# Kernel tuning notes

Measured on AMD Instinct MI355X. Metric: run time of the kernel, lower is better.

The kernel has to match this reference:

```python
import jax, jax.numpy as jnp
import numpy as np

B, T, D_MODEL, N_HEADS = 2, 2048, 2048, 16
D_HEAD = D_MODEL // N_HEADS
SCALE = 1.0 / np.sqrt(D_HEAD)


def setup_inputs() -> dict:
    key = jax.random.key(0)
    ks = jax.random.split(key, 5)
    w_std = 1.0 / np.sqrt(D_MODEL)
    x = jax.random.normal(ks[0], (B, T, D_MODEL), dtype=jnp.float32)
    W_q = jax.random.normal(ks[1], (D_MODEL, D_MODEL), dtype=jnp.float32) * w_std
    W_k = jax.random.normal(ks[2], (D_MODEL, D_MODEL), dtype=jnp.float32) * w_std
    W_v = jax.random.normal(ks[3], (D_MODEL, D_MODEL), dtype=jnp.float32) * w_std
    W_o = jax.random.normal(ks[4], (D_MODEL, D_MODEL), dtype=jnp.float32) * w_std
    return {"x": x, "W_q": W_q, "W_k": W_k, "W_v": W_v, "W_o": W_o}


def _split_heads(y):
    # [B, T, D] -> [B, H, T, d_head]
    b, t, _ = y.shape
    return y.reshape(b, t, N_HEADS, D_HEAD).transpose(0, 2, 1, 3)


def reference(x, W_q, W_k, W_v, W_o):
    # Linear layers (torch nn.Linear: y = x @ W.T)
    Q = _split_heads(x @ W_q.T)
    K = _split_heads(x @ W_k.T)
    V = _split_heads(x @ W_v.T)
    # Causal softmax attention (math-equivalent to the tiled online-softmax loop)
    scores = jnp.einsum('bhqd,bhkd->bhqk', Q, K) * SCALE
    causal_mask = jnp.tril(jnp.ones((T, T), dtype=bool))  # [T, T]
    scores = jnp.where(causal_mask, scores, -jnp.inf)
    P = jax.nn.softmax(scores, axis=-1)
    O = jnp.einsum('bhqk,bhkd->bhqd', P, V)
    out = O.transpose(0, 2, 1, 3).reshape(B, T, D_MODEL)  # merge heads
    return out @ W_o.T
```

## Files before the change

kernel.cpp:

```cpp
#include <hip/hip_runtime.h>
#include <hip/hip_bf16.h>
#include <hip/hip_fp16.h>

#define B_   2
#define T_   2048
#define DM   2048
#define NH   16
#define DH   128
#define M_   (B_*T_)
#define SCALE_ 0.08838834764831845f

typedef _Float16 f16;
typedef f16  half8 __attribute__((ext_vector_type(8)));
typedef f16  half4 __attribute__((ext_vector_type(4)));
typedef float f32x4 __attribute__((ext_vector_type(4)));

#define GL16(gp, lp) __builtin_amdgcn_global_load_lds( \
    (const __attribute__((address_space(1))) void*)(gp), \
    (__attribute__((address_space(3))) void*)(lp), 16, 0, 0)

#define MFMA16(a, b, c) __builtin_amdgcn_mfma_f32_16x16x32_f16((a), (b), (c), 0, 0, 0)

struct CvtArgs { const float* s[5]; f16* d[5]; };

__global__ __launch_bounds__(256) void convert_all(CvtArgs a) {
    size_t i4 = (size_t)blockIdx.x * 256 + threadIdx.x;
    int r; size_t off;
    if (i4 < 2097152) { r = 0; off = i4; }
    else { size_t k = i4 - 2097152; r = 1 + (int)(k >> 20); off = k & 1048575; }
    float4 v = *((const float4*)a.s[r] + off);
    half4 h;
    h[0] = (f16)v.x; h[1] = (f16)v.y; h[2] = (f16)v.z; h[3] = (f16)v.w;
    *((half4*)a.d[r] + off) = h;
}

#define NT_K 32

__global__ __launch_bounds__(512, 2)
void qkv3(const f16* __restrict__ A, const f16* __restrict__ Bw,
          f16* __restrict__ dst)
{
    __shared__ __align__(16) char smem[114688];

    const int tid  = threadIdx.x;
    const int lane = tid & 63;
    const int w    = tid >> 6;
    const int wr   = w >> 1, wc = w & 1;

    const int id = (blockIdx.x & 7) * 64 + (blockIdx.x >> 3);
    const int bm = id & 15, bn = id >> 4;
    const int m0 = bm * 256, n0 = bn * 192;

    const int scol8 = (((tid & 7) ^ ((tid >> 3) & 7)) << 3);
    const int rc0 = (((lane >> 4) * 16)      ) ^ ((lane & 7) << 4);
    const int rc1 = (64 + (lane >> 4) * 16   ) ^ ((lane & 7) << 4);

    f32x4 acc[4][6] = {};

#define QSTAGE_A(bufb, ch, s, kt) GL16( \
    A + (size_t)(m0 + (ch)*128 + (tid>>8)*64 + (s)*32 + ((tid>>3)&31)) * 2048 + (kt)*64 + scol8, \
    smem + (bufb)*57344 + (ch)*16384 + (s)*8192 + w*1024)
#define QSTAGE_B(bufb, u, kt) GL16( \
    Bw + (size_t)(n0 + (tid>>7)*48 + (u)*16 + ((tid>>3)&15)) * 2048 + (kt)*64 + scol8, \
    smem + (bufb)*57344 + 32768 + (u)*8192 + w*1024)

    const int abase = (wr >> 1) * 16384 + (wr & 1) * 4096 + (lane & 15) * 128;
    const int bbase = 32768 + wc * 4096 + (lane & 15) * 128;

    half8 af0[4][2], af1[4][2], bnx[2];

    QSTAGE_A(0, 0, 0, 0); QSTAGE_A(0, 0, 1, 0);
    QSTAGE_A(0, 1, 0, 0); QSTAGE_A(0, 1, 1, 0);
    QSTAGE_B(0, 0, 0);    QSTAGE_B(0, 1, 0);    QSTAGE_B(0, 2, 0);
    {
        asm volatile("s_waitcnt vmcnt(2)" ::: "memory");
        __builtin_amdgcn_s_barrier();
        __builtin_amdgcn_sched_barrier(0);
        const char* buf0 = smem;
        #pragma unroll
        for (int m = 0; m < 4; ++m) {
            const char* p = buf0 + (m >> 1) * 8192 + abase + (m & 1) * 2048;
            af0[m][0] = *(const half8*)(p + rc0);
            af0[m][1] = *(const half8*)(p + rc1);
        }
        bnx[0] = *(const half8*)(buf0 + bbase + rc0);
        bnx[1] = *(const half8*)(buf0 + bbase + rc1);
    }

#define GATE(n_) do { \
    asm volatile("s_waitcnt vmcnt(" #n_ ")" ::: "memory"); \
    __builtin_amdgcn_s_barrier(); \
    __builtin_amdgcn_sched_barrier(0); \
} while (0)

#define MFC(AF, BB, f_) do { \
    __builtin_amdgcn_s_setprio(1); \
    _Pragma("unroll") \
    for (int m_ = 0; m_ < 4; ++m_) { \
        acc[m_][f_] = MFMA16(AF[m_][0], (BB)[0], acc[m_][f_]); \
        acc[m_][f_] = MFMA16(AF[m_][1], (BB)[1], acc[m_][f_]); \
    } \
    __builtin_amdgcn_s_setprio(0); \
} while (0)

#define RDB(dstv, off) do { \
    const char* p_ = buf + bbase + (off); \
    dstv[0] = *(const half8*)(p_ + rc0); \
    dstv[1] = *(const half8*)(p_ + rc1); \
} while (0)

#define BODY(t_, c_, AFC, AFN) do { \
    const char* buf  = smem + (c_) * 57344; \
    const char* nbuf = smem + ((c_) ^ 1) * 57344; \
    const int  kt    = ((t_) + 1 < NT_K) ? (t_) + 1 : (t_); \
    half8 b3[2], b1[2], b4[2], b2[2], b5[2]; \
     \
    RDB(b3, 2048); \
    QSTAGE_A((c_) ^ 1, 0, 0, kt); QSTAGE_A((c_) ^ 1, 0, 1, kt); \
    MFC(AFC, bnx, 0); \
     \
    GATE(3); \
    RDB(b1, 8192); \
    QSTAGE_A((c_) ^ 1, 1, 0, kt); QSTAGE_A((c_) ^ 1, 1, 1, kt); \
    MFC(AFC, b3, 3); \
     \
    RDB(b4, 8192 + 2048); \
    QSTAGE_B((c_) ^ 1, 0, kt); \
    MFC(AFC, b1, 1); \
     \
    GATE(5); \
    RDB(b2, 16384); \
    QSTAGE_B((c_) ^ 1, 1, kt); \
    MFC(AFC, b4, 4); \
     \
    GATE(1); \
    RDB(b5, 16384 + 2048); \
    { const char* p_ = nbuf + abase; \
      AFN[0][0] = *(const half8*)(p_ + rc0); \
      AFN[0][1] = *(const half8*)(p_ + rc1); \
      AFN[1][0] = *(const half8*)(p_ + 2048 + rc0); \
      AFN[1][1] = *(const half8*)(p_ + 2048 + rc1); } \
    QSTAGE_B((c_) ^ 1, 2, kt); \
    MFC(AFC, b2, 2); \
     \
    { const char* p_ = nbuf + 8192 + abase; \
      AFN[2][0] = *(const half8*)(p_ + rc0); \
      AFN[2][1] = *(const half8*)(p_ + rc1); \
      AFN[3][0] = *(const half8*)(p_ + 2048 + rc0); \
      AFN[3][1] = *(const half8*)(p_ + 2048 + rc1); } \
    { const char* p_ = nbuf + bbase; \
      bnx[0] = *(const half8*)(p_ + rc0); \
      bnx[1] = *(const half8*)(p_ + rc1); } \
    MFC(AFC, b5, 5); \
} while (0)

    for (int t = 0; t < NT_K; t += 2) {
        BODY(t,     0, af0, af1);
        BODY(t + 1, 1, af1, af0);
    }
#undef BODY
#undef RDB
#undef MFC
#undef GATE
#undef QSTAGE_A
#undef QSTAGE_B

    asm volatile("s_waitcnt vmcnt(0)" ::: "memory");

    #pragma unroll
    for (int m = 0; m < 4; ++m)
        #pragma unroll
        for (int f = 0; f < 6; ++f)
            #pragma unroll
            for (int j = 0; j < 4; ++j) {
                int row  = m0 + wr * 64 + m * 16 + (lane >> 4) * 4 + j;
                int gcol = n0 + wc * 96 + f * 16 + (lane & 15);
                int sec = gcol >> 11, cic = gcol & 2047;
                int b = row >> 11, tt = row & (T_ - 1);
                int h = cic >> 7, d = cic & 127;
                float cs = (sec == 0) ? SCALE_ : 1.0f;
                dst[(size_t)sec * ((size_t)M_ * 2048) +
                    ((size_t)(b * NH + h) * T_ + tt) * DH + d] = (f16)(acc[m][f][j] * cs);
            }
}

#define NT_W 32

__global__ __launch_bounds__(512, 2)
void wo2(const f16* __restrict__ A, const f16* __restrict__ Bw,
         float* __restrict__ Cf)
{
    __shared__ __align__(16) char smem[98304];

    const int tid  = threadIdx.x;
    const int lane = tid & 63;
    const int w    = tid >> 6;
    const int wr   = w >> 1, wc = w & 1;

    const int id = (blockIdx.x & 7) * 32 + (blockIdx.x >> 3);
    const int bm = id & 15, bn = id >> 4;
    const int m0 = bm * 256, n0 = bn * 128;

    const int scol8 = (((tid & 7) ^ ((tid >> 3) & 7)) << 3);
    const int rc0 = (((lane >> 4) * 16)      ) ^ ((lane & 7) << 4);
    const int rc1 = (64 + (lane >> 4) * 16   ) ^ ((lane & 7) << 4);

    f32x4 acc[4][4] = {};

#define WSA(bufb, s, kt) GL16( \
    A + (size_t)(m0 + ((s)&1)*128 + (tid>>8)*64 + ((s)>>1)*32 + ((tid>>3)&31)) * 2048 + (kt)*64 + scol8, \
    smem + (bufb)*49152 + (s)*8192 + w*1024)
#define WSB(bufb, u, kt) GL16( \
    Bw + (size_t)(n0 + (tid>>8)*64 + (u)*32 + ((tid>>3)&31)) * 2048 + (kt)*64 + scol8, \
    smem + (bufb)*49152 + 32768 + (u)*8192 + w*1024)

    WSA(0, 0, 0); WSA(0, 1, 0); WSB(0, 0, 0); WSB(0, 1, 0);
    WSA(0, 2, 0); WSA(0, 3, 0);

    const int abase = (wr >> 1) * 8192 + (wr & 1) * 4096 + (lane & 15) * 128;
    const int bbase = 32768 + wc * 4096 + (lane & 15) * 128;

#define WGATE(n_) do { \
    asm volatile("s_waitcnt vmcnt(" #n_ ")" ::: "memory"); \
    __builtin_amdgcn_s_barrier(); \
    __builtin_amdgcn_sched_barrier(0); \
} while (0)

    for (int t = 0; t < NT_W; ++t) {
        const int c = t & 1;
        const char* buf = smem + c * 49152;
        const int kt = (t + 1 < NT_W) ? t + 1 : t;

        half8 af[4][2], bf[4][2];

        WGATE(2);
        #pragma unroll
        for (int m = 0; m < 2; ++m) {
            const char* p = buf + abase + m * 2048;
            af[m][0] = *(const half8*)(p + rc0);
            af[m][1] = *(const half8*)(p + rc1);
        }
        #pragma unroll
        for (int n = 0; n < 4; ++n) {
            const char* p = buf + bbase + (n >> 1) * 8192 + (n & 1) * 2048;
            bf[n][0] = *(const half8*)(p + rc0);
            bf[n][1] = *(const half8*)(p + rc1);
        }
        WSA(c ^ 1, 0, kt); WSA(c ^ 1, 1, kt);
        WSB(c ^ 1, 0, kt); WSB(c ^ 1, 1, kt);
        __builtin_amdgcn_s_setprio(1);
        #pragma unroll
        for (int m = 0; m < 2; ++m)
            #pragma unroll
            for (int n = 0; n < 4; ++n) {
                acc[m][n] = MFMA16(af[m][0], bf[n][0], acc[m][n]);
                acc[m][n] = MFMA16(af[m][1], bf[n][1], acc[m][n]);
            }
        __builtin_amdgcn_s_setprio(0);

        WGATE(4);
        #pragma unroll
        for (int m = 2; m < 4; ++m) {
            const char* p = buf + 16384 + abase + (m & 1) * 2048;
            af[m][0] = *(const half8*)(p + rc0);
            af[m][1] = *(const half8*)(p + rc1);
        }
        WSA(c ^ 1, 2, kt); WSA(c ^ 1, 3, kt);
        __builtin_amdgcn_s_setprio(1);
        #pragma unroll
        for (int m = 2; m < 4; ++m)
            #pragma unroll
            for (int n = 0; n < 4; ++n) {
                acc[m][n] = MFMA16(af[m][0], bf[n][0], acc[m][n]);
                acc[m][n] = MFMA16(af[m][1], bf[n][1], acc[m][n]);
            }
        __builtin_amdgcn_s_setprio(0);
    }
#undef WGATE
#undef WSA
#undef WSB

    asm volatile("s_waitcnt vmcnt(0)" ::: "memory");

    #pragma unroll
    for (int m = 0; m < 4; ++m)
        #pragma unroll
        for (int n = 0; n < 4; ++n)
            #pragma unroll
            for (int j = 0; j < 4; ++j) {
                int row = m0 + wr * 64 + m * 16 + (lane >> 4) * 4 + j;
                int col = n0 + wc * 64 + n * 16 + (lane & 15);
                Cf[(size_t)row * 2048 + col] = acc[m][n][j];
            }
}

__global__ __launch_bounds__(256)
void vtrans(const f16* __restrict__ Vin, f16* __restrict__ Vout)
{
    __shared__ f16 ld[64][72];
    const int tid = threadIdx.x;
    const int dd = blockIdx.x;
    const int tt = blockIdx.y;
    const int bh = blockIdx.z;

    const int r  = tid >> 2;
    const int s2 = (tid & 3) * 2;

    const f16* src = Vin + ((size_t)bh * T_ + tt * 64 + r) * DH + dd * 64;
    half8 v0 = *(const half8*)(src + s2 * 8);
    half8 v1 = *(const half8*)(src + s2 * 8 + 8);
    #pragma unroll
    for (int e = 0; e < 8; ++e) ld[s2 * 8 + e][r]     = v0[e];
    #pragma unroll
    for (int e = 0; e < 8; ++e) ld[s2 * 8 + 8 + e][r] = v1[e];
    __syncthreads();

    f16* dst = Vout + ((size_t)bh * DH + dd * 64 + r) * T_ + tt * 64;
    *(half8*)(dst + s2 * 8)     = *(const half8*)&ld[r][s2 * 8];
    *(half8*)(dst + s2 * 8 + 8) = *(const half8*)&ld[r][s2 * 8 + 8];
}

#define QB 64
#define KB 64
#define PP 72
#define NQT (T_/QB)

__global__ __launch_bounds__(256, 2)
void attn_fwd(const f16* __restrict__ Q, const f16* __restrict__ K,
              const f16* __restrict__ Vt, f16* __restrict__ O)
{
    __shared__ __align__(16) char Ks[2][16384];
    __shared__ __align__(16) char Vs[2][16384];
    __shared__ __align__(16) f16 Ps[4][16][PP];

    const int tid  = threadIdx.x;
    const int lane = tid & 63;
    const int w    = tid >> 6;
    const int g    = lane >> 4;

    const int bid  = blockIdx.x;
    const int swz  = (bid & 7) * 64 + (bid >> 3);
    const int bh   = swz >> 4;
    const int pair = swz & 15;
    const size_t base = (size_t)bh * T_ * DH;
    const int b = bh >> 4, h = bh & 15;

    const int krow0 = w * 4 + g;
    const int kswz  = ((lane & 15) ^ (krow0 & 7)) << 3;
    const int vrow0 = w * 8 + (lane >> 3);
    const int vswz  = (((lane & 7) ^ ((lane >> 3) & 7)) << 3);

#define STAGE_K(c_, kv) do { \
    _Pragma("unroll") for (int i_ = 0; i_ < 4; ++i_) { \
        const f16* g_ = K + base + (size_t)((kv) + i_*16 + krow0) * DH + kswz; \
        GL16(g_, &Ks[c_][i_*4096 + w*1024]); } } while (0)
#define STAGE_V(c_, kv) do { \
    _Pragma("unroll") for (int i_ = 0; i_ < 4; ++i_) { \
        const f16* g_ = Vt + base + (size_t)(i_*32 + vrow0) * T_ + (kv) + vswz; \
        GL16(g_, &Vs[c_][i_*4096 + w*1024]); } } while (0)

#define QKT(SA, QF) do { \
    __builtin_amdgcn_s_setprio(1); \
    _Pragma("unroll") \
    for (int n_ = 0; n_ < 4; ++n_) \
        _Pragma("unroll") \
        for (int kk_ = 0; kk_ < 4; ++kk_) { \
            half8 kfv = *(const half8*)(kb + (n_*16 + (lane & 15)) * 256 + \
                ((kk_*32 + g * 8) * 2 ^ ((lane & 7) << 4))); \
            SA[n_] = MFMA16(kfv, QF[kk_], SA[n_]); \
        } \
    __builtin_amdgcn_s_setprio(0); \
} while (0)

#define SMAX(SA, MRUN, LSUM, OO) do { \
    float mx_ = SA[0][0]; \
    _Pragma("unroll") \
    for (int n_ = 0; n_ < 4; ++n_) \
        _Pragma("unroll") \
        for (int j_ = 0; j_ < 4; ++j_) mx_ = fmaxf(mx_, SA[n_][j_]); \
    mx_ = fmaxf(mx_, __shfl_xor(mx_, 16)); \
    mx_ = fmaxf(mx_, __shfl_xor(mx_, 32)); \
    if (!__all(mx_ <= MRUN + 5.f)) { \
        float mnew_ = fmaxf(MRUN, mx_); \
        float sf_ = __expf(MRUN - mnew_); \
        _Pragma("unroll") \
        for (int nn_ = 0; nn_ < 8; ++nn_) OO[nn_] *= sf_; \
        LSUM *= sf_; \
        MRUN = mnew_; \
    } \
    float rs_ = 0.f; \
    _Pragma("unroll") \
    for (int n_ = 0; n_ < 4; ++n_) \
        _Pragma("unroll") \
        for (int j_ = 0; j_ < 4; ++j_) { \
            float p_ = __expf(SA[n_][j_] - MRUN); \
            SA[n_][j_] = p_; \
            rs_ += p_; \
        } \
    LSUM += rs_; \
} while (0)

#define PFRAG(SA, BP) do { \
    _Pragma("unroll") \
    for (int n_ = 0; n_ < 4; ++n_) { \
        half4 hv_; \
        hv_[0] = (f16)SA[n_][0]; hv_[1] = (f16)SA[n_][1]; \
        hv_[2] = (f16)SA[n_][2]; hv_[3] = (f16)SA[n_][3]; \
        *reinterpret_cast<half4*>(&Ps[w][lane & 15][n_*16 + g*4]) = hv_; \
    } \
    _Pragma("unroll") \
    for (int cc_ = 0; cc_ < 2; ++cc_) \
        BP[cc_] = *reinterpret_cast<const half8*>(&Ps[w][lane & 15][cc_*32 + g*8]); \
} while (0)

#define PV(OO, BP) do { \
    __builtin_amdgcn_s_setprio(1); \
    _Pragma("unroll") \
    for (int n_ = 0; n_ < 8; ++n_) \
        _Pragma("unroll") \
        for (int cc_ = 0; cc_ < 2; ++cc_) { \
            half8 vf_ = *(const half8*)(vb + (n_*16 + (lane & 15)) * 128 + \
                ((cc_*64 + g*16) ^ ((lane & 7) << 4))); \
            OO[n_] = MFMA16(vf_, BP[cc_], OO[n_]); \
        } \
    __builtin_amdgcn_s_setprio(0); \
} while (0)

    const int qt1 = pair;
    const int qt2 = NQT - 1 - pair;
    const int nt1 = qt1 + 1;
    const int ntU = qt2 + 1;
    const int qg1 = qt1 * QB + w * 16 + (lane & 15);
    const int qg2 = qt2 * QB + w * 16 + (lane & 15);

    half8 qf1[4], qf2[4];
    #pragma unroll
    for (int kk = 0; kk < 4; ++kk) {
        qf1[kk] = *reinterpret_cast<const half8*>(
            &Q[base + (size_t)qg1 * DH + kk * 32 + g * 8]);
        qf2[kk] = *reinterpret_cast<const half8*>(
            &Q[base + (size_t)qg2 * DH + kk * 32 + g * 8]);
    }

    float mrun1 = -1e30f, lsum1 = 0.f;
    float mrun2 = -1e30f, lsum2 = 0.f;
    f32x4 o1[8] = {};
    f32x4 o2[8] = {};

    STAGE_K(0, 0);
    STAGE_V(0, 0);

    for (int it = 0; it < ntU; ++it) {
        const int c = it & 1;
        __syncthreads();
        if (it + 1 < ntU) {
            STAGE_K(c ^ 1, (it + 1) * KB);
            STAGE_V(c ^ 1, (it + 1) * KB);
        }
        const bool s1 = (it < nt1);
        const char* kb = &Ks[c][0];
        const char* vb = &Vs[c][0];

        f32x4 sa2[4] = {};
        f32x4 sa1[4] = {};

        QKT(sa2, qf2);
        if (s1) QKT(sa1, qf1);

        if (it == ntU - 1) {
            #pragma unroll
            for (int n = 0; n < 4; ++n)
                #pragma unroll
                for (int j = 0; j < 4; ++j) {
                    int kg = it * KB + n*16 + g*4 + j;
                    if (kg > qg2) sa2[n][j] = -1e30f;
                }
        }
        if (s1 && it == nt1 - 1) {
            #pragma unroll
            for (int n = 0; n < 4; ++n)
                #pragma unroll
                for (int j = 0; j < 4; ++j) {
                    int kg = it * KB + n*16 + g*4 + j;
                    if (kg > qg1) sa1[n][j] = -1e30f;
                }
        }

        SMAX(sa2, mrun2, lsum2, o2);
        half8 bp2[2];
        PFRAG(sa2, bp2);
        PV(o2, bp2);

        if (s1) {
            SMAX(sa1, mrun1, lsum1, o1);
            half8 bp1[2];
            PFRAG(sa1, bp1);
            PV(o1, bp1);
        }
    }

    {
        float l2 = lsum2;
        l2 += __shfl_xor(l2, 16);
        l2 += __shfl_xor(l2, 32);
        float invl = 1.0f / l2;
        #pragma unroll
        for (int n = 0; n < 8; ++n) {
            half4 hv;
            hv[0] = (f16)(o2[n][0] * invl); hv[1] = (f16)(o2[n][1] * invl);
            hv[2] = (f16)(o2[n][2] * invl); hv[3] = (f16)(o2[n][3] * invl);
            *reinterpret_cast<half4*>(
                &O[((size_t)(b * T_ + qg2) * NH + h) * DH + n*16 + g*4]) = hv;
        }
    }
    {
        float l1 = lsum1;
        l1 += __shfl_xor(l1, 16);
        l1 += __shfl_xor(l1, 32);
        float invl = 1.0f / l1;
        #pragma unroll
        for (int n = 0; n < 8; ++n) {
            half4 hv;
            hv[0] = (f16)(o1[n][0] * invl); hv[1] = (f16)(o1[n][1] * invl);
            hv[2] = (f16)(o1[n][2] * invl); hv[3] = (f16)(o1[n][3] * invl);
            *reinterpret_cast<half4*>(
                &O[((size_t)(b * T_ + qg1) * NH + h) * DH + n*16 + g*4]) = hv;
        }
    }
#undef PV
#undef PFRAG
#undef SMAX
#undef QKT
#undef STAGE_K
#undef STAGE_V
}

extern "C" void kernel_launch(void* const* d_in, const int* in_sizes, int n_in,
                              void* d_out, int out_size, void* d_ws, size_t ws_size,
                              hipStream_t stream)
{
    const float* x  = (const float*)d_in[0];
    const float* wq = (const float*)d_in[1];
    const float* wk = (const float*)d_in[2];
    const float* wv = (const float*)d_in[3];
    const float* wo = (const float*)d_in[4];
    float* out = (float*)d_out;

    const size_t nx = (size_t)M_ * DM;
    const size_t nw = (size_t)DM * DM;
    const size_t need = (nx * 5 + nw * 4) * sizeof(f16);
    if (ws_size < need) return;

    char* ws = (char*)d_ws;
    f16* xh  = (f16*)ws;  ws += nx * 2;
    f16* wqh = (f16*)ws;  ws += nw * 2;
    f16* wkh = (f16*)ws;  ws += nw * 2;
    f16* wvh = (f16*)ws;  ws += nw * 2;
    f16* woh = (f16*)ws;  ws += nw * 2;
    f16* Qh  = (f16*)ws;  ws += nx * 2;
    f16* Kh  = (f16*)ws;  ws += nx * 2;
    f16* Vh  = (f16*)ws;  ws += nx * 2;
    f16* Oh  = (f16*)ws;  ws += nx * 2;

    f16* Vth = xh;

    CvtArgs ca;
    ca.s[0] = x;  ca.d[0] = xh;
    ca.s[1] = wq; ca.d[1] = wqh;
    ca.s[2] = wk; ca.d[2] = wkh;
    ca.s[3] = wv; ca.d[3] = wvh;
    ca.s[4] = wo; ca.d[4] = woh;
    convert_all<<<24576, 256, 0, stream>>>(ca);

    qkv3<<<dim3(512), 512, 0, stream>>>(xh, wqh, Qh);

    vtrans<<<dim3(2, 32, 32), 256, 0, stream>>>(Vh, Vth);

    attn_fwd<<<dim3(512), 256, 0, stream>>>(Qh, Kh, Vth, Oh);

    wo2<<<dim3(256), 512, 0, stream>>>(Oh, woh, out);
}
```

Before: 228.4 us.

## Share K/V LDS fragment loads across paired query tiles; shrink Wo GEMM tiles

In attention, the two query tiles handled by a block now share each K and V fragment read from LDS, issuing both MFMAs per load instead of reading the fragments twice. The Wo projection GEMM moves from 256x128 tiles with 512 threads to 128x128 tiles with 256 threads over 512 blocks, with smaller LDS buffers and adjusted wait counts. The attention change cuts LDS traffic but raises register pressure. The Wo change trades per-block reuse for more blocks and possibly higher occupancy.

```diff
diff --git a/kernel.cpp b/kernel.cpp
--- a/kernel.cpp
+++ b/kernel.cpp
@@ -186,20 +186,20 @@
 
 #define NT_W 32
 
-__global__ __launch_bounds__(512, 2)
+__global__ __launch_bounds__(256, 2)
 void wo2(const f16* __restrict__ A, const f16* __restrict__ Bw,
          float* __restrict__ Cf)
 {
-    __shared__ __align__(16) char smem[98304];
+    __shared__ __align__(16) char smem[65536];
 
     const int tid  = threadIdx.x;
     const int lane = tid & 63;
     const int w    = tid >> 6;
     const int wr   = w >> 1, wc = w & 1;
 
-    const int id = (blockIdx.x & 7) * 32 + (blockIdx.x >> 3);
-    const int bm = id & 15, bn = id >> 4;
-    const int m0 = bm * 256, n0 = bn * 128;
+    const int id = (blockIdx.x & 7) * 64 + (blockIdx.x >> 3);
+    const int bm = id & 31, bn = id >> 5;
+    const int m0 = bm * 128, n0 = bn * 128;
 
     const int scol8 = (((tid & 7) ^ ((tid >> 3) & 7)) << 3);
     const int rc0 = (((lane >> 4) * 16)      ) ^ ((lane & 7) << 4);
@@ -208,17 +208,18 @@
     f32x4 acc[4][4] = {};
 
 #define WSA(bufb, s, kt) GL16( \
-    A + (size_t)(m0 + ((s)&1)*128 + (tid>>8)*64 + ((s)>>1)*32 + ((tid>>3)&31)) * 2048 + (kt)*64 + scol8, \
-    smem + (bufb)*49152 + (s)*8192 + w*1024)
+    A + (size_t)(m0 + ((s)&1)*64 + ((s)>>1)*32 + (tid>>3)) * 2048 + (kt)*64 + scol8, \
+    smem + (bufb)*32768 + (s)*4096 + w*1024)
 #define WSB(bufb, u, kt) GL16( \
-    Bw + (size_t)(n0 + (tid>>8)*64 + (u)*32 + ((tid>>3)&31)) * 2048 + (kt)*64 + scol8, \
-    smem + (bufb)*49152 + 32768 + (u)*8192 + w*1024)
-
-    WSA(0, 0, 0); WSA(0, 1, 0); WSB(0, 0, 0); WSB(0, 1, 0);
+    Bw + (size_t)(n0 + ((u)&1)*64 + ((u)>>1)*32 + (tid>>3)) * 2048 + (kt)*64 + scol8, \
+    smem + (bufb)*32768 + 16384 + (u)*4096 + w*1024)
+
+    WSA(0, 0, 0); WSA(0, 1, 0);
+    WSB(0, 0, 0); WSB(0, 1, 0); WSB(0, 2, 0); WSB(0, 3, 0);
     WSA(0, 2, 0); WSA(0, 3, 0);
 
-    const int abase = (wr >> 1) * 8192 + (wr & 1) * 4096 + (lane & 15) * 128;
-    const int bbase = 32768 + wc * 4096 + (lane & 15) * 128;
+    const int abase = wr * 4096 + (lane & 15) * 128;
+    const int bbase = 16384 + wc * 4096 + (lane & 15) * 128;
 
 #define WGATE(n_) do { \
     asm volatile("s_waitcnt vmcnt(" #n_ ")" ::: "memory"); \
@@ -228,7 +229,7 @@
 
     for (int t = 0; t < NT_W; ++t) {
         const int c = t & 1;
-        const char* buf = smem + c * 49152;
+        const char* buf = smem + c * 32768;
         const int kt = (t + 1 < NT_W) ? t + 1 : t;
 
         half8 af[4][2], bf[4][2];
@@ -236,7 +237,7 @@
         WGATE(2);
         #pragma unroll
         for (int m = 0; m < 2; ++m) {
-            const char* p = buf + abase + m * 2048;
+            const char* p = buf + abase + (m & 1) * 2048;
             af[m][0] = *(const half8*)(p + rc0);
             af[m][1] = *(const half8*)(p + rc1);
         }
@@ -247,7 +248,7 @@
             bf[n][1] = *(const half8*)(p + rc1);
         }
         WSA(c ^ 1, 0, kt); WSA(c ^ 1, 1, kt);
-        WSB(c ^ 1, 0, kt); WSB(c ^ 1, 1, kt);
+        WSB(c ^ 1, 0, kt); WSB(c ^ 1, 1, kt); WSB(c ^ 1, 2, kt); WSB(c ^ 1, 3, kt);
         __builtin_amdgcn_s_setprio(1);
         #pragma unroll
         for (int m = 0; m < 2; ++m)
@@ -258,10 +259,10 @@
             }
         __builtin_amdgcn_s_setprio(0);
 
-        WGATE(4);
+        WGATE(6);
         #pragma unroll
         for (int m = 2; m < 4; ++m) {
-            const char* p = buf + 16384 + abase + (m & 1) * 2048;
+            const char* p = buf + 8192 + abase + (m & 1) * 2048;
             af[m][0] = *(const half8*)(p + rc0);
             af[m][1] = *(const half8*)(p + rc1);
         }
@@ -358,19 +359,6 @@
     _Pragma("unroll") for (int i_ = 0; i_ < 4; ++i_) { \
         const f16* g_ = Vt + base + (size_t)(i_*32 + vrow0) * T_ + (kv) + vswz; \
         GL16(g_, &Vs[c_][i_*4096 + w*1024]); } } while (0)
-
-#define QKT(SA, QF) do { \
-    __builtin_amdgcn_s_setprio(1); \
-    _Pragma("unroll") \
-    for (int n_ = 0; n_ < 4; ++n_) \
-        _Pragma("unroll") \
-        for (int kk_ = 0; kk_ < 4; ++kk_) { \
-            half8 kfv = *(const half8*)(kb + (n_*16 + (lane & 15)) * 256 + \
-                ((kk_*32 + g * 8) * 2 ^ ((lane & 7) << 4))); \
-            SA[n_] = MFMA16(kfv, QF[kk_], SA[n_]); \
-        } \
-    __builtin_amdgcn_s_setprio(0); \
-} while (0)
 
 #define SMAX(SA, MRUN, LSUM, OO) do { \
     float mx_ = SA[0][0]; \
@@ -413,19 +401,6 @@
         BP[cc_] = *reinterpret_cast<const half8*>(&Ps[w][lane & 15][cc_*32 + g*8]); \
 } while (0)
 
-#define PV(OO, BP) do { \
-    __builtin_amdgcn_s_setprio(1); \
-    _Pragma("unroll") \
-    for (int n_ = 0; n_ < 8; ++n_) \
-        _Pragma("unroll") \
-        for (int cc_ = 0; cc_ < 2; ++cc_) { \
-            half8 vf_ = *(const half8*)(vb + (n_*16 + (lane & 15)) * 128 + \
-                ((cc_*64 + g*16) ^ ((lane & 7) << 4))); \
-            OO[n_] = MFMA16(vf_, BP[cc_], OO[n_]); \
-        } \
-    __builtin_amdgcn_s_setprio(0); \
-} while (0)
-
     const int qt1 = pair;
     const int qt2 = NQT - 1 - pair;
     const int nt1 = qt1 + 1;
@@ -464,8 +439,28 @@
         f32x4 sa2[4] = {};
         f32x4 sa1[4] = {};
 
-        QKT(sa2, qf2);
-        if (s1) QKT(sa1, qf1);
+        __builtin_amdgcn_s_setprio(1);
+        if (s1) {
+            #pragma unroll
+            for (int n = 0; n < 4; ++n)
+                #pragma unroll
+                for (int kk = 0; kk < 4; ++kk) {
+                    half8 kfv = *(const half8*)(kb + (n*16 + (lane & 15)) * 256 +
+                        ((kk*32 + g * 8) * 2 ^ ((lane & 7) << 4)));
+                    sa2[n] = MFMA16(kfv, qf2[kk], sa2[n]);
+                    sa1[n] = MFMA16(kfv, qf1[kk], sa1[n]);
+                }
+        } else {
+            #pragma unroll
+            for (int n = 0; n < 4; ++n)
+                #pragma unroll
+                for (int kk = 0; kk < 4; ++kk) {
+                    half8 kfv = *(const half8*)(kb + (n*16 + (lane & 15)) * 256 +
+                        ((kk*32 + g * 8) * 2 ^ ((lane & 7) << 4)));
+                    sa2[n] = MFMA16(kfv, qf2[kk], sa2[n]);
+                }
+        }
+        __builtin_amdgcn_s_setprio(0);
 
         if (it == ntU - 1) {
             #pragma unroll
@@ -487,16 +482,35 @@
         }
 
         SMAX(sa2, mrun2, lsum2, o2);
-        half8 bp2[2];
-        PFRAG(sa2, bp2);
-        PV(o2, bp2);
-
+        half8 bp2[2], bp1[2];
         if (s1) {
             SMAX(sa1, mrun1, lsum1, o1);
-            half8 bp1[2];
             PFRAG(sa1, bp1);
-            PV(o1, bp1);
-        }
+        }
+        PFRAG(sa2, bp2);
+
+        __builtin_amdgcn_s_setprio(1);
+        if (s1) {
+            #pragma unroll
+            for (int n = 0; n < 8; ++n)
+                #pragma unroll
+                for (int cc = 0; cc < 2; ++cc) {
+                    half8 vf = *(const half8*)(vb + (n*16 + (lane & 15)) * 128 +
+                        ((cc*64 + g*16) ^ ((lane & 7) << 4)));
+                    o2[n] = MFMA16(vf, bp2[cc], o2[n]);
+                    o1[n] = MFMA16(vf, bp1[cc], o1[n]);
+                }
+        } else {
+            #pragma unroll
+            for (int n = 0; n < 8; ++n)
+                #pragma unroll
+                for (int cc = 0; cc < 2; ++cc) {
+                    half8 vf = *(const half8*)(vb + (n*16 + (lane & 15)) * 128 +
+                        ((cc*64 + g*16) ^ ((lane & 7) << 4)));
+                    o2[n] = MFMA16(vf, bp2[cc], o2[n]);
+                }
+        }
+        __builtin_amdgcn_s_setprio(0);
     }
 
     {
@@ -527,10 +541,8 @@
                 &O[((size_t)(b * T_ + qg1) * NH + h) * DH + n*16 + g*4]) = hv;
         }
     }
-#undef PV
 #undef PFRAG
 #undef SMAX
-#undef QKT
 #undef STAGE_K
 #undef STAGE_V
 }
@@ -578,5 +590,5 @@
 
     attn_fwd<<<dim3(512), 256, 0, stream>>>(Qh, Kh, Vth, Oh);
 
-    wo2<<<dim3(256), 512, 0, stream>>>(Oh, woh, out);
+    wo2<<<dim3(512), 256, 0, stream>>>(Oh, woh, out);
 }
```

Result: slower. 233.2 us (+2.1%).
